# Optimization experiments

Hardware: AMD Instinct MI355X
Metric: run time of the kernel (lower is better)

The kernel has to match this reference:

```python
import jax, jax.numpy as jnp
import numpy as np
import math

D = 256; H = 8; DH = 32; FF = 2048; L = 6; B = 4; S = 1022


def _pe(n, d):
    pos = np.arange(n)[:, None]
    div = np.exp(np.arange(0, d, 2) * (-math.log(10000.0) / d))
    pe = np.zeros((n, d), np.float32)
    pe[:, 0::2] = np.sin(pos * div)
    pe[:, 1::2] = np.cos(pos * div)
    return jnp.asarray(pe)


def _ln(x, g, b):
    mu = x.mean(-1, keepdims=True)
    v = ((x - mu) ** 2).mean(-1, keepdims=True)
    return (x - mu) / jnp.sqrt(v + 1e-5) * g + b


def _forward(x, cls1, cls2, Wqkv, bqkv, Wo, bo, ln1_g, ln1_b, W1, b1, W2, b2, ln2_g, ln2_b, idx, pad):
    n = x.shape[1] + 2  # insert cls1 and cls2 tokens
    h = jnp.stack([jnp.concatenate([cls1, x[i, :idx[i]], cls2, x[i, idx[i]:]], axis=0) for i in range(B)])
    h = h + _pe(n, D)[None]  # [B,N,D]
    # block-diagonal two-segment mask per sample (additive bias form)
    pos = np.arange(n)
    bias = []
    for i in range(B):
        v1 = pos <= idx[i]
        v2 = (pos > idx[i]) & (pos < n - pad[i])
        allowed = np.outer(v1, v1) | np.outer(v2, v2)
        bias.append(np.where(allowed, 0.0, -1e9).astype(np.float32))
    bias = jnp.asarray(np.stack(bias))[:, None]  # [B,1,N,N]
    scale = 1.0 / math.sqrt(DH)
    for l in range(L):
        qkv = h @ Wqkv[l].T + bqkv[l]  # [B,N,3D]
        q, k, v = jnp.split(qkv, 3, axis=-1)
        q = q.reshape(B, n, H, DH).transpose(0, 2, 1, 3)
        k = k.reshape(B, n, H, DH).transpose(0, 2, 1, 3)
        v = v.reshape(B, n, H, DH).transpose(0, 2, 1, 3)
        scores = jnp.einsum('bhqd,bhkd->bhqk', q, k) * scale + bias
        p = jax.nn.softmax(scores, axis=-1)
        a = jnp.einsum('bhqk,bhkd->bhqd', p, v).transpose(0, 2, 1, 3).reshape(B, n, D)
        h = _ln(h + a @ Wo[l].T + bo[l], ln1_g[l], ln1_b[l])
        ff = jax.nn.relu(h @ W1[l].T + b1[l]) @ W2[l].T + b2[l]
        h = _ln(h + ff, ln2_g[l], ln2_b[l])
    # cls token outputs: position 0 (cls1) and position idx+1 (cls2)
    return jnp.stack([jnp.stack([h[i, 0], h[i, idx[i] + 1]]) for i in range(B)])  # [4,2,256]


def setup_inputs():
    key = jax.random.key(0)
    ks = jax.random.split(key, 8)
    s = 0.02
    return {
        'x': jax.random.normal(ks[0], (B, S, D), jnp.float32),
        'mask': jnp.zeros((1,), jnp.bool_),  # unused by the original forward
        'indices': jnp.array([[500, 600, 400, 300], [0, 0, 0, 0]], jnp.int32),
        'cls1': jax.random.uniform(ks[1], (1, D), jnp.float32),
        'cls2': jax.random.uniform(ks[2], (1, D), jnp.float32),
        'Wqkv': jax.random.normal(ks[3], (L, 3 * D, D), jnp.float32) * s,
        'bqkv': jnp.zeros((L, 3 * D), jnp.float32),
        'Wo': jax.random.normal(ks[4], (L, D, D), jnp.float32) * s,
        'bo': jnp.zeros((L, D), jnp.float32),
        'ln1_g': jnp.ones((L, D), jnp.float32),
        'ln1_b': jnp.zeros((L, D), jnp.float32),
        'W1': jax.random.normal(ks[5], (L, FF, D), jnp.float32) * s,
        'b1': jnp.zeros((L, FF), jnp.float32),
        'W2': jax.random.normal(ks[6], (L, D, FF), jnp.float32) * s,
        'b2': jnp.zeros((L, D), jnp.float32),
        'ln2_g': jnp.ones((L, D), jnp.float32),
        'ln2_b': jnp.zeros((L, D), jnp.float32),
    }


def reference(x, mask, indices, cls1, cls2, Wqkv, bqkv, Wo, bo, ln1_g, ln1_b, W1, b1, W2, b2, ln2_g, ln2_b):
    ind = np.asarray(indices)
    idx = [int(t) for t in ind[0]]
    pad = [int(t) for t in ind[1]]
    return _forward(x, cls1, cls2, Wqkv, bqkv, Wo, bo, ln1_g, ln1_b, W1, b1, W2, b2, ln2_g, ln2_b, idx, pad)
```

## Files before the change

kernel.cpp:

```cpp
#include <hip/hip_runtime.h>
#include <hip/hip_bf16.h>
#include <math.h>

typedef __hip_bfloat16 bf16;
typedef short bf16x8 __attribute__((ext_vector_type(8)));
typedef short short4v __attribute__((ext_vector_type(4)));
typedef float f32x4 __attribute__((ext_vector_type(4)));

#define D_MODEL 256
#define NTOK 1024
#define SEQ 1022
#define BATCH 4
#define NLAYER 6

__device__ inline void gload_lds16(const void* g, void* l) {
    __builtin_amdgcn_global_load_lds(
        (const __attribute__((address_space(1))) void*)g,
        (__attribute__((address_space(3))) void*)l, 16, 0, 0);
}

__global__ __launch_bounds__(256) void cast4_kernel(
    const float* __restrict__ s0, bf16* __restrict__ d0,
    const float* __restrict__ s1, bf16* __restrict__ d1,
    const float* __restrict__ s2, bf16* __restrict__ d2,
    const float* __restrict__ s3, bf16* __restrict__ d3)
{
    const int bid = blockIdx.x;
    const float* s; bf16* d; int base;
    if (bid < 1152)      { s = s0; d = d0; base = bid; }
    else if (bid < 1536) { s = s1; d = d1; base = bid - 1152; }
    else if (bid < 4608) { s = s2; d = d2; base = bid - 1536; }
    else                 { s = s3; d = d3; base = bid - 4608; }
    const int i = (base * 256 + threadIdx.x) * 4;
    f32x4 v = *(const f32x4*)(s + i);
    d[i + 0] = __float2bfloat16(v[0]);
    d[i + 1] = __float2bfloat16(v[1]);
    d[i + 2] = __float2bfloat16(v[2]);
    d[i + 3] = __float2bfloat16(v[3]);
}

__global__ __launch_bounds__(256) void embed_kernel(
    const float* __restrict__ x, const float* __restrict__ cls1,
    const float* __restrict__ cls2, const int* __restrict__ ind,
    float* __restrict__ h, bf16* __restrict__ hb)
{
    int i = blockIdx.x * 256 + threadIdx.x;
    int d = i & 255;
    int pos = (i >> 8) & 1023;
    int b = i >> 18;
    int idx = ind[b];
    float v;
    if (pos == 0) v = cls1[d];
    else if (pos == idx + 1) v = cls2[d];
    else if (pos <= idx) v = x[(b * SEQ + pos - 1) * D_MODEL + d];
    else v = x[(b * SEQ + pos - 2) * D_MODEL + d];
    int p = d >> 1;
    float freq = expf(-(float)p * (logf(10000.0f) / 128.0f));
    float ang = (float)pos * freq;
    v += (d & 1) ? cosf(ang) : sinf(ang);
    h[i] = v;
    hb[i] = __float2bfloat16(v);
}

template<int MR, int NR, int RELU, int HAS_RES, int WF32, int WBF16, int WVT, int SPLITK>
__global__ __launch_bounds__(256) void mfma_gemm(
    const bf16* __restrict__ A, const bf16* __restrict__ W,
    const float* __restrict__ bias, const float* __restrict__ R,
    float* __restrict__ Cf, bf16* __restrict__ Cb, bf16* __restrict__ vTb,
    int M, int N, int K)
{
    constexpr int BM = MR * 32, BN = NR * 32;
    constexpr int ACH = BM * 4;
    constexpr int BCH = BN * 4;
    __shared__ bf16 As[2][BM * 32];
    __shared__ bf16 Bs[2][BN * 32];
    const int ntile = N / BN;
    const int tiles = (M / BM) * ntile;
    const int ks = (SPLITK > 1) ? (blockIdx.x / tiles) : 0;
    const int bidt = (SPLITK > 1) ? (blockIdx.x % tiles) : blockIdx.x;
    const int bx = bidt % ntile, by = bidt / ntile;
    const int row0 = by * BM, col0 = bx * BN;
    const int KS = K / SPLITK;
    const int kbase = ks * KS;
    const int tid = threadIdx.x, lane = tid & 63, wave = tid >> 6;
    const int wr = wave >> 1, wc = wave & 1;
    const int l15 = lane & 15, l4 = lane >> 4;

    f32x4 acc[MR][NR];
    #pragma unroll
    for (int m = 0; m < MR; ++m)
        #pragma unroll
        for (int n = 0; n < NR; ++n) acc[m][n] = (f32x4)0.0f;

    const int nk = KS / 32;

    auto stage = [&](int buf, int t) {
        const int k0 = kbase + t * 32;
        #pragma unroll
        for (int p = 0; p < ACH / 256; ++p) {
            const int cbase = p * 256 + wave * 64;
            const int chunk = cbase + lane;
            const int r = chunk >> 2, c = chunk & 3;
            gload_lds16(A + (size_t)(row0 + r) * K + k0 + c * 8, &As[buf][cbase * 8]);
        }
        #pragma unroll
        for (int p = 0; p < BCH / 256; ++p) {
            const int cbase = p * 256 + wave * 64;
            const int chunk = cbase + lane;
            const int r = chunk >> 2, c = chunk & 3;
            gload_lds16(W + (size_t)(col0 + r) * K + k0 + c * 8, &Bs[buf][cbase * 8]);
        }
    };

    stage(0, 0);
    __syncthreads();
    int cur = 0;
    for (int t = 0; t < nk; ++t) {
        if (t + 1 < nk) stage(cur ^ 1, t + 1);
        bf16x8 af[MR], bfr[NR];
        #pragma unroll
        for (int m = 0; m < MR; ++m)
            af[m] = *(const bf16x8*)&As[cur][(wr * MR * 16 + m * 16 + l15) * 32 + l4 * 8];
        #pragma unroll
        for (int n = 0; n < NR; ++n)
            bfr[n] = *(const bf16x8*)&Bs[cur][(wc * NR * 16 + n * 16 + l15) * 32 + l4 * 8];
        #pragma unroll
        for (int m = 0; m < MR; ++m)
            #pragma unroll
            for (int n = 0; n < NR; ++n)
                acc[m][n] = __builtin_amdgcn_mfma_f32_16x16x32_bf16(af[m], bfr[n], acc[m][n], 0, 0, 0);
        __syncthreads();
        cur ^= 1;
    }

    #pragma unroll
    for (int m = 0; m < MR; ++m) {
        #pragma unroll
        for (int n = 0; n < NR; ++n) {
            const int col = col0 + wc * NR * 16 + n * 16 + l15;
            const float bv = (SPLITK > 1) ? 0.0f : bias[col];
            #pragma unroll
            for (int r = 0; r < 4; ++r) {
                const int row = row0 + wr * MR * 16 + m * 16 + l4 * 4 + r;
                float v = acc[m][n][r] + bv;
                if (HAS_RES) v += R[(size_t)row * N + col];
                if (RELU) v = fmaxf(v, 0.0f);
                if (WF32) Cf[(size_t)ks * M * N + (size_t)row * N + col] = v;
                if (WBF16) {
                    if (WVT && col >= 512) {
                        const int hh = (col >> 5) - 16, d = col & 31;
                        const int bb = row >> 10, tt = row & 1023;
                        vTb[(((size_t)bb * 8 + hh) * 32 + d) * 1024 + tt] = __float2bfloat16(v);
                    } else {
                        Cb[(size_t)row * N + col] = __float2bfloat16(v);
                    }
                }
            }
        }
    }
}

template<int K>
__global__ __launch_bounds__(512) void gemm256_ln8_kernel(
    const bf16* __restrict__ A, const bf16* __restrict__ W,
    const float* __restrict__ bias, const float* __restrict__ g,
    const float* __restrict__ be, float* __restrict__ h, bf16* __restrict__ hb)
{
    constexpr int KW = K / 8;
    constexpr int NSTEP = KW / 32;
    __shared__ float part[4][16][260];
    const int tid = threadIdx.x, lane = tid & 63, wave = tid >> 6;
    const int l15 = lane & 15, l4 = lane >> 4;
    const int row0 = blockIdx.x * 16;

    f32x4 acc[16];
    #pragma unroll
    for (int n = 0; n < 16; ++n) acc[n] = (f32x4)0.0f;
    #pragma unroll
    for (int s = 0; s < NSTEP; ++s) {
        const int kk = wave * KW + s * 32;
        const bf16x8 af = *(const bf16x8*)(A + (size_t)(row0 + l15) * K + kk + l4 * 8);
        #pragma unroll
        for (int n = 0; n < 16; ++n) {
            const bf16x8 bfr = *(const bf16x8*)(W + (size_t)(n * 16 + l15) * K + kk + l4 * 8);
            acc[n] = __builtin_amdgcn_mfma_f32_16x16x32_bf16(af, bfr, acc[n], 0, 0, 0);
        }
    }
    if (wave < 4) {
        #pragma unroll
        for (int n = 0; n < 16; ++n)
            #pragma unroll
            for (int r = 0; r < 4; ++r)
                part[wave][l4 * 4 + r][n * 16 + l15] = acc[n][r];
    }
    __syncthreads();
    if (wave >= 4) {
        #pragma unroll
        for (int n = 0; n < 16; ++n)
            #pragma unroll
            for (int r = 0; r < 4; ++r)
                part[wave - 4][l4 * 4 + r][n * 16 + l15] += acc[n][r];
    }
    __syncthreads();

    const int row = tid >> 5, c8 = (tid & 31) * 8;
    f32x4 v0 = *(const f32x4*)&part[0][row][c8];
    f32x4 v1 = *(const f32x4*)&part[0][row][c8 + 4];
    #pragma unroll
    for (int w = 1; w < 4; ++w) {
        v0 += *(const f32x4*)&part[w][row][c8];
        v1 += *(const f32x4*)&part[w][row][c8 + 4];
    }
    float* hrow = h + (size_t)(row0 + row) * 256 + c8;
    v0 += *(const f32x4*)(bias + c8)     + *(const f32x4*)(hrow);
    v1 += *(const f32x4*)(bias + c8 + 4) + *(const f32x4*)(hrow + 4);
    float s1 = (v0[0] + v0[1]) + (v0[2] + v0[3]) + (v1[0] + v1[1]) + (v1[2] + v1[3]);
    #pragma unroll
    for (int off = 16; off >= 1; off >>= 1) s1 += __shfl_xor(s1, off);
    const float mu = s1 * (1.0f / 256.0f);
    float s2 = 0.0f;
    #pragma unroll
    for (int q = 0; q < 4; ++q) { float d0 = v0[q] - mu, d1 = v1[q] - mu; s2 += d0 * d0 + d1 * d1; }
    #pragma unroll
    for (int off = 16; off >= 1; off >>= 1) s2 += __shfl_xor(s2, off);
    const float inv = 1.0f / sqrtf(s2 * (1.0f / 256.0f) + 1e-5f);
    short* hbrow = (short*)hb + (size_t)(row0 + row) * 256 + c8;
    const f32x4 gv0 = *(const f32x4*)(g + c8),  gv1 = *(const f32x4*)(g + c8 + 4);
    const f32x4 ev0 = *(const f32x4*)(be + c8), ev1 = *(const f32x4*)(be + c8 + 4);
    f32x4 y0, y1; short4v p0, p1;
    #pragma unroll
    for (int q = 0; q < 4; ++q) {
        y0[q] = (v0[q] - mu) * inv * gv0[q] + ev0[q];
        y1[q] = (v1[q] - mu) * inv * gv1[q] + ev1[q];
        p0[q] = __builtin_bit_cast(short, __float2bfloat16(y0[q]));
        p1[q] = __builtin_bit_cast(short, __float2bfloat16(y1[q]));
    }
    *(f32x4*)(hrow) = y0;  *(f32x4*)(hrow + 4) = y1;
    *(short4v*)(hbrow) = p0;  *(short4v*)(hbrow + 4) = p1;
}

__global__ __launch_bounds__(256) void ln_merge_kernel(
    const float* __restrict__ P0, const float* __restrict__ P1,
    const float* __restrict__ bias, const float* __restrict__ g,
    const float* __restrict__ bb, float* __restrict__ h, bf16* __restrict__ hb)
{
    const int row = blockIdx.x * 4 + (threadIdx.x >> 6);
    const int lane = threadIdx.x & 63;
    const size_t off = (size_t)row * 256 + lane * 4;
    f32x4 xv = *(const f32x4*)(P0 + off);
    xv += *(const f32x4*)(P1 + off);
    xv += *(const f32x4*)(bias + lane * 4);
    xv += *(const f32x4*)(h + off);
    float s = (xv[0] + xv[1]) + (xv[2] + xv[3]);
    #pragma unroll
    for (int o = 32; o >= 1; o >>= 1) s += __shfl_xor(s, o);
    const float mu = s * (1.0f / 256.0f);
    f32x4 dv;
    float s2 = 0.0f;
    #pragma unroll
    for (int e = 0; e < 4; ++e) { dv[e] = xv[e] - mu; s2 += dv[e] * dv[e]; }
    #pragma unroll
    for (int o = 32; o >= 1; o >>= 1) s2 += __shfl_xor(s2, o);
    const float inv = 1.0f / sqrtf(s2 * (1.0f / 256.0f) + 1e-5f);
    const f32x4 gv = *(const f32x4*)(g + lane * 4);
    const f32x4 bv = *(const f32x4*)(bb + lane * 4);
    f32x4 y;
    short4v pk;
    #pragma unroll
    for (int e = 0; e < 4; ++e) {
        y[e] = dv[e] * inv * gv[e] + bv[e];
        pk[e] = __builtin_bit_cast(short, __float2bfloat16(y[e]));
    }
    *(f32x4*)(h + off) = y;
    *(short4v*)((short*)hb + off) = pk;
}

__global__ __launch_bounds__(256) void attn_mfma_kernel(
    const bf16* __restrict__ qkvb, const bf16* __restrict__ vT,
    bf16* __restrict__ att, const int* __restrict__ ind)
{
    __shared__ bf16 Ps[4][16][72];
    __shared__ float Opart[4][64][8];
    __shared__ float MLpart[4][64][8];
    const int qt = blockIdx.x & 31;
    const int hh = (blockIdx.x >> 5) & 7;
    const int b  = blockIdx.x >> 8;
    const int idx = ind[b];
    const int segEnd = NTOK - ind[4 + b];
    const int tid = threadIdx.x, lane = tid & 63, wave = tid >> 6;
    const int strip = wave >> 1, kh = wave & 1;
    const int l15 = lane & 15, l4 = lane >> 4;
    const int q0 = qt * 32 + strip * 16;
    const size_t tokbase = (size_t)b * NTOK;
    const bf16* vTh = vT + (((size_t)b * 8 + hh) * 32) * 1024;
    const float scale = 0.17677669529663687f;

    const bf16x8 qfrag = *(const bf16x8*)(qkvb + (tokbase + q0 + l15) * 768 + hh * 32 + l4 * 8);

    f32x4 acc_o[2];
    acc_o[0] = (f32x4)0.0f; acc_o[1] = (f32x4)0.0f;
    float mrun[4], lrun[4];
    bool v1q[4], v2q[4];
    #pragma unroll
    for (int r = 0; r < 4; ++r) {
        mrun[r] = -1e30f; lrun[r] = 0.0f;
        const int qg = q0 + l4 * 4 + r;
        v1q[r] = (qg <= idx);
        v2q[r] = (qg > idx) && (qg < segEnd);
    }

    const int kbeg = (q0 <= idx) ? 0 : (idx + 1);
    const int kend = (q0 + 15 > idx) ? segEnd : (idx + 1);
    const int t0 = kbeg & ~63;
    const int T = (kend - t0 + 63) >> 6;
    const int i0 = kh ? (T >> 1) : 0;
    const int i1 = kh ? T : (T >> 1);

    for (int i = i0; i < i1; ++i) {
        const int k0 = t0 + (i << 6);
        f32x4 sc[4];
        #pragma unroll
        for (int kt = 0; kt < 4; ++kt) {
            const bf16x8 kf = *(const bf16x8*)
                (qkvb + (tokbase + k0 + kt * 16 + l15) * 768 + 256 + hh * 32 + l4 * 8);
            sc[kt] = __builtin_amdgcn_mfma_f32_16x16x32_bf16(qfrag, kf, (f32x4)0.0f, 0, 0, 0);
        }
        float mloc[4] = {-1e30f, -1e30f, -1e30f, -1e30f};
        #pragma unroll
        for (int kt = 0; kt < 4; ++kt) {
            const int k = k0 + kt * 16 + l15;
            const bool v1k = (k <= idx);
            const bool v2k = (k > idx) && (k < segEnd);
            #pragma unroll
            for (int r = 0; r < 4; ++r) {
                const bool ok = (v1q[r] && v1k) || (v2q[r] && v2k);
                const float s = ok ? sc[kt][r] * scale : -1e30f;
                sc[kt][r] = s;
                mloc[r] = fmaxf(mloc[r], s);
            }
        }
        #pragma unroll
        for (int r = 0; r < 4; ++r) {
            mloc[r] = fmaxf(mloc[r], __shfl_xor(mloc[r], 1));
            mloc[r] = fmaxf(mloc[r], __shfl_xor(mloc[r], 2));
            mloc[r] = fmaxf(mloc[r], __shfl_xor(mloc[r], 4));
            mloc[r] = fmaxf(mloc[r], __shfl_xor(mloc[r], 8));
            const float mnew = fmaxf(mrun[r], mloc[r]);
            const float c = __expf(mrun[r] - mnew);
            mrun[r] = mnew;
            mloc[r] = c;
        }
        float psum[4] = {0.0f, 0.0f, 0.0f, 0.0f};
        #pragma unroll
        for (int kt = 0; kt < 4; ++kt) {
            #pragma unroll
            for (int r = 0; r < 4; ++r) {
                const float s = sc[kt][r];
                const float p = (s > -5e29f) ? __expf(s - mrun[r]) : 0.0f;
                psum[r] += p;
                Ps[wave][l4 * 4 + r][kt * 16 + l15] = __float2bfloat16(p);
            }
        }
        #pragma unroll
        for (int r = 0; r < 4; ++r) {
            float ps = psum[r];
            ps += __shfl_xor(ps, 1); ps += __shfl_xor(ps, 2);
            ps += __shfl_xor(ps, 4); ps += __shfl_xor(ps, 8);
            lrun[r] = lrun[r] * mloc[r] + ps;
            acc_o[0][r] *= mloc[r];
            acc_o[1][r] *= mloc[r];
        }
        #pragma unroll
        for (int ks = 0; ks < 2; ++ks) {
            const bf16x8 pa = *(const bf16x8*)&Ps[wave][l15][ks * 32 + l4 * 8];
            #pragma unroll
            for (int dt = 0; dt < 2; ++dt) {
                const bf16x8 vb = *(const bf16x8*)
                    (vTh + (size_t)(dt * 16 + l15) * 1024 + k0 + ks * 32 + l4 * 8);
                acc_o[dt] = __builtin_amdgcn_mfma_f32_16x16x32_bf16(pa, vb, acc_o[dt], 0, 0, 0);
            }
        }
    }

    #pragma unroll
    for (int r = 0; r < 4; ++r) {
        Opart[wave][lane][r]     = acc_o[0][r];
        Opart[wave][lane][4 + r] = acc_o[1][r];
        MLpart[wave][lane][r]     = mrun[r];
        MLpart[wave][lane][4 + r] = lrun[r];
    }
    __syncthreads();
    if (kh == 0) {
        #pragma unroll
        for (int r = 0; r < 4; ++r) {
            const float m1 = MLpart[wave + 1][lane][r];
            const float l1 = MLpart[wave + 1][lane][4 + r];
            const float ms = fmaxf(mrun[r], m1);
            const float c0 = __expf(mrun[r] - ms);
            const float c1 = __expf(m1 - ms);
            const float lt = lrun[r] * c0 + l1 * c1;
            const float invl = (lt > 0.0f) ? (1.0f / lt) : 0.0f;
            const float o0 = (acc_o[0][r] * c0 + Opart[wave + 1][lane][r] * c1) * invl;
            const float o1 = (acc_o[1][r] * c0 + Opart[wave + 1][lane][4 + r] * c1) * invl;
            const int qg = q0 + l4 * 4 + r;
            bf16* op = att + (tokbase + qg) * 256 + hh * 32 + l15;
            op[0]  = __float2bfloat16(o0);
            op[16] = __float2bfloat16(o1);
        }
    }
}

__global__ __launch_bounds__(256) void gather_kernel(
    const float* __restrict__ h, const int* __restrict__ ind, float* __restrict__ out)
{
    int b = blockIdx.x;
    int tid = threadIdx.x;
    out[(b * 2 + 0) * 256 + tid] = h[(b * NTOK + 0) * 256 + tid];
    out[(b * 2 + 1) * 256 + tid] = h[(b * NTOK + ind[b] + 1) * 256 + tid];
}

extern "C" void kernel_launch(void* const* d_in, const int* in_sizes, int n_in,
                              void* d_out, int out_size, void* d_ws, size_t ws_size,
                              hipStream_t stream)
{
    const float* x    = (const float*)d_in[0];
    const int*   ind  = (const int*)d_in[2];
    const float* cls1 = (const float*)d_in[3];
    const float* cls2 = (const float*)d_in[4];
    const float* Wqkv = (const float*)d_in[5];
    const float* bqkv = (const float*)d_in[6];
    const float* Wo   = (const float*)d_in[7];
    const float* bo   = (const float*)d_in[8];
    const float* g1   = (const float*)d_in[9];
    const float* be1  = (const float*)d_in[10];
    const float* W1   = (const float*)d_in[11];
    const float* bf1  = (const float*)d_in[12];
    const float* W2   = (const float*)d_in[13];
    const float* bf2  = (const float*)d_in[14];
    const float* g2   = (const float*)d_in[15];
    const float* be2  = (const float*)d_in[16];
    float* out = (float*)d_out;

    float* ws   = (float*)d_ws;
    float* h    = ws;
    float* tmp2 = h + 1048576;
    bf16* hb    = (bf16*)(tmp2 + 2097152);
    bf16* qkvb  = hb + 1048576;
    bf16* vTb   = qkvb + 3145728;
    bf16* attb  = vTb + 1048576;
    bf16* ffb   = attb + 1048576;
    bf16* wqkvb = ffb + 8388608;
    bf16* wob   = wqkvb + 1179648;
    bf16* w1b   = wob + 393216;
    bf16* w2b   = w1b + 3145728;

    const int M = BATCH * NTOK;

    cast4_kernel<<<7680, 256, 0, stream>>>(Wqkv, wqkvb, Wo, wob, W1, w1b, W2, w2b);
    embed_kernel<<<M, 256, 0, stream>>>(x, cls1, cls2, ind, h, hb);

    for (int l = 0; l < NLAYER; ++l) {
        const bf16*  Wqkv_l = wqkvb + (size_t)l * 196608;
        const float* bqkv_l = bqkv + (size_t)l * 768;
        const bf16*  Wo_l   = wob + (size_t)l * 65536;
        const float* bo_l   = bo + (size_t)l * 256;
        const float* g1_l   = g1 + (size_t)l * 256;
        const float* be1_l  = be1 + (size_t)l * 256;
        const bf16*  W1_l   = w1b + (size_t)l * 524288;
        const float* b1_l   = bf1 + (size_t)l * 2048;
        const bf16*  W2_l   = w2b + (size_t)l * 524288;
        const float* b2_l   = bf2 + (size_t)l * 256;
        const float* g2_l   = g2 + (size_t)l * 256;
        const float* be2_l  = be2 + (size_t)l * 256;

        mfma_gemm<2, 4, 0, 0, 0, 1, 1, 1><<<(M / 64) * (768 / 128), 256, 0, stream>>>(
            hb, Wqkv_l, bqkv_l, nullptr, nullptr, qkvb, vTb, M, 768, 256);
        attn_mfma_kernel<<<BATCH * 8 * 32, 256, 0, stream>>>(qkvb, vTb, attb, ind);
        gemm256_ln8_kernel<256><<<M / 16, 512, 0, stream>>>(
            attb, Wo_l, bo_l, g1_l, be1_l, h, hb);
        mfma_gemm<4, 4, 1, 0, 0, 1, 0, 1><<<(M / 128) * (2048 / 128), 256, 0, stream>>>(
            hb, W1_l, b1_l, nullptr, nullptr, ffb, nullptr, M, 2048, 256);
        mfma_gemm<2, 2, 0, 0, 1, 0, 0, 2><<<2 * (M / 64) * (256 / 64), 256, 0, stream>>>(
            ffb, W2_l, nullptr, nullptr, tmp2, nullptr, nullptr, M, 256, 2048);
        ln_merge_kernel<<<M / 4, 256, 0, stream>>>(
            tmp2, tmp2 + (size_t)M * 256, b2_l, g2_l, be2_l, h, hb);
    }

    gather_kernel<<<BATCH, 256, 0, stream>>>(h, ind, out);
}
```

Before: 485.9 us.

## Fuse attention with Wo projection and LayerNorm into one kernel

```diff
diff --git a/kernel.cpp b/kernel.cpp
--- a/kernel.cpp
+++ b/kernel.cpp
@@ -160,137 +160,22 @@
     }
 }
 
-template<int K>
-__global__ __launch_bounds__(512) void gemm256_ln8_kernel(
-    const bf16* __restrict__ A, const bf16* __restrict__ W,
-    const float* __restrict__ bias, const float* __restrict__ g,
-    const float* __restrict__ be, float* __restrict__ h, bf16* __restrict__ hb)
-{
-    constexpr int KW = K / 8;
-    constexpr int NSTEP = KW / 32;
+__global__ __launch_bounds__(512) void attn_wo_ln_kernel(
+    const bf16* __restrict__ qkvb, const bf16* __restrict__ vT,
+    const bf16* __restrict__ Wo, const float* __restrict__ bo,
+    const float* __restrict__ g, const float* __restrict__ be,
+    float* __restrict__ h, bf16* __restrict__ hb, const int* __restrict__ ind)
+{
+    __shared__ bf16 Ps[8][16][72];
+    __shared__ bf16 att_s[16][264];
     __shared__ float part[4][16][260];
-    const int tid = threadIdx.x, lane = tid & 63, wave = tid >> 6;
-    const int l15 = lane & 15, l4 = lane >> 4;
-    const int row0 = blockIdx.x * 16;
-
-    f32x4 acc[16];
-    #pragma unroll
-    for (int n = 0; n < 16; ++n) acc[n] = (f32x4)0.0f;
-    #pragma unroll
-    for (int s = 0; s < NSTEP; ++s) {
-        const int kk = wave * KW + s * 32;
-        const bf16x8 af = *(const bf16x8*)(A + (size_t)(row0 + l15) * K + kk + l4 * 8);
-        #pragma unroll
-        for (int n = 0; n < 16; ++n) {
-            const bf16x8 bfr = *(const bf16x8*)(W + (size_t)(n * 16 + l15) * K + kk + l4 * 8);
-            acc[n] = __builtin_amdgcn_mfma_f32_16x16x32_bf16(af, bfr, acc[n], 0, 0, 0);
-        }
-    }
-    if (wave < 4) {
-        #pragma unroll
-        for (int n = 0; n < 16; ++n)
-            #pragma unroll
-            for (int r = 0; r < 4; ++r)
-                part[wave][l4 * 4 + r][n * 16 + l15] = acc[n][r];
-    }
-    __syncthreads();
-    if (wave >= 4) {
-        #pragma unroll
-        for (int n = 0; n < 16; ++n)
-            #pragma unroll
-            for (int r = 0; r < 4; ++r)
-                part[wave - 4][l4 * 4 + r][n * 16 + l15] += acc[n][r];
-    }
-    __syncthreads();
-
-    const int row = tid >> 5, c8 = (tid & 31) * 8;
-    f32x4 v0 = *(const f32x4*)&part[0][row][c8];
-    f32x4 v1 = *(const f32x4*)&part[0][row][c8 + 4];
-    #pragma unroll
-    for (int w = 1; w < 4; ++w) {
-        v0 += *(const f32x4*)&part[w][row][c8];
-        v1 += *(const f32x4*)&part[w][row][c8 + 4];
-    }
-    float* hrow = h + (size_t)(row0 + row) * 256 + c8;
-    v0 += *(const f32x4*)(bias + c8)     + *(const f32x4*)(hrow);
-    v1 += *(const f32x4*)(bias + c8 + 4) + *(const f32x4*)(hrow + 4);
-    float s1 = (v0[0] + v0[1]) + (v0[2] + v0[3]) + (v1[0] + v1[1]) + (v1[2] + v1[3]);
-    #pragma unroll
-    for (int off = 16; off >= 1; off >>= 1) s1 += __shfl_xor(s1, off);
-    const float mu = s1 * (1.0f / 256.0f);
-    float s2 = 0.0f;
-    #pragma unroll
-    for (int q = 0; q < 4; ++q) { float d0 = v0[q] - mu, d1 = v1[q] - mu; s2 += d0 * d0 + d1 * d1; }
-    #pragma unroll
-    for (int off = 16; off >= 1; off >>= 1) s2 += __shfl_xor(s2, off);
-    const float inv = 1.0f / sqrtf(s2 * (1.0f / 256.0f) + 1e-5f);
-    short* hbrow = (short*)hb + (size_t)(row0 + row) * 256 + c8;
-    const f32x4 gv0 = *(const f32x4*)(g + c8),  gv1 = *(const f32x4*)(g + c8 + 4);
-    const f32x4 ev0 = *(const f32x4*)(be + c8), ev1 = *(const f32x4*)(be + c8 + 4);
-    f32x4 y0, y1; short4v p0, p1;
-    #pragma unroll
-    for (int q = 0; q < 4; ++q) {
-        y0[q] = (v0[q] - mu) * inv * gv0[q] + ev0[q];
-        y1[q] = (v1[q] - mu) * inv * gv1[q] + ev1[q];
-        p0[q] = __builtin_bit_cast(short, __float2bfloat16(y0[q]));
-        p1[q] = __builtin_bit_cast(short, __float2bfloat16(y1[q]));
-    }
-    *(f32x4*)(hrow) = y0;  *(f32x4*)(hrow + 4) = y1;
-    *(short4v*)(hbrow) = p0;  *(short4v*)(hbrow + 4) = p1;
-}
-
-__global__ __launch_bounds__(256) void ln_merge_kernel(
-    const float* __restrict__ P0, const float* __restrict__ P1,
-    const float* __restrict__ bias, const float* __restrict__ g,
-    const float* __restrict__ bb, float* __restrict__ h, bf16* __restrict__ hb)
-{
-    const int row = blockIdx.x * 4 + (threadIdx.x >> 6);
-    const int lane = threadIdx.x & 63;
-    const size_t off = (size_t)row * 256 + lane * 4;
-    f32x4 xv = *(const f32x4*)(P0 + off);
-    xv += *(const f32x4*)(P1 + off);
-    xv += *(const f32x4*)(bias + lane * 4);
-    xv += *(const f32x4*)(h + off);
-    float s = (xv[0] + xv[1]) + (xv[2] + xv[3]);
-    #pragma unroll
-    for (int o = 32; o >= 1; o >>= 1) s += __shfl_xor(s, o);
-    const float mu = s * (1.0f / 256.0f);
-    f32x4 dv;
-    float s2 = 0.0f;
-    #pragma unroll
-    for (int e = 0; e < 4; ++e) { dv[e] = xv[e] - mu; s2 += dv[e] * dv[e]; }
-    #pragma unroll
-    for (int o = 32; o >= 1; o >>= 1) s2 += __shfl_xor(s2, o);
-    const float inv = 1.0f / sqrtf(s2 * (1.0f / 256.0f) + 1e-5f);
-    const f32x4 gv = *(const f32x4*)(g + lane * 4);
-    const f32x4 bv = *(const f32x4*)(bb + lane * 4);
-    f32x4 y;
-    short4v pk;
-    #pragma unroll
-    for (int e = 0; e < 4; ++e) {
-        y[e] = dv[e] * inv * gv[e] + bv[e];
-        pk[e] = __builtin_bit_cast(short, __float2bfloat16(y[e]));
-    }
-    *(f32x4*)(h + off) = y;
-    *(short4v*)((short*)hb + off) = pk;
-}
-
-__global__ __launch_bounds__(256) void attn_mfma_kernel(
-    const bf16* __restrict__ qkvb, const bf16* __restrict__ vT,
-    bf16* __restrict__ att, const int* __restrict__ ind)
-{
-    __shared__ bf16 Ps[4][16][72];
-    __shared__ float Opart[4][64][8];
-    __shared__ float MLpart[4][64][8];
-    const int qt = blockIdx.x & 31;
-    const int hh = (blockIdx.x >> 5) & 7;
-    const int b  = blockIdx.x >> 8;
+    const int qt = blockIdx.x & 63;
+    const int b  = blockIdx.x >> 6;
     const int idx = ind[b];
     const int segEnd = NTOK - ind[4 + b];
-    const int tid = threadIdx.x, lane = tid & 63, wave = tid >> 6;
-    const int strip = wave >> 1, kh = wave & 1;
+    const int tid = threadIdx.x, lane = tid & 63, hh = tid >> 6;
     const int l15 = lane & 15, l4 = lane >> 4;
-    const int q0 = qt * 32 + strip * 16;
+    const int q0 = qt * 16;
     const size_t tokbase = (size_t)b * NTOK;
     const bf16* vTh = vT + (((size_t)b * 8 + hh) * 32) * 1024;
     const float scale = 0.17677669529663687f;
@@ -311,13 +196,8 @@
 
     const int kbeg = (q0 <= idx) ? 0 : (idx + 1);
     const int kend = (q0 + 15 > idx) ? segEnd : (idx + 1);
-    const int t0 = kbeg & ~63;
-    const int T = (kend - t0 + 63) >> 6;
-    const int i0 = kh ? (T >> 1) : 0;
-    const int i1 = kh ? T : (T >> 1);
-
-    for (int i = i0; i < i1; ++i) {
-        const int k0 = t0 + (i << 6);
+
+    for (int k0 = (kbeg & ~63); k0 < kend; k0 += 64) {
         f32x4 sc[4];
         #pragma unroll
         for (int kt = 0; kt < 4; ++kt) {
@@ -358,7 +238,7 @@
                 const float s = sc[kt][r];
                 const float p = (s > -5e29f) ? __expf(s - mrun[r]) : 0.0f;
                 psum[r] += p;
-                Ps[wave][l4 * 4 + r][kt * 16 + l15] = __float2bfloat16(p);
+                Ps[hh][l4 * 4 + r][kt * 16 + l15] = __float2bfloat16(p);
             }
         }
         #pragma unroll
@@ -372,7 +252,7 @@
         }
         #pragma unroll
         for (int ks = 0; ks < 2; ++ks) {
-            const bf16x8 pa = *(const bf16x8*)&Ps[wave][l15][ks * 32 + l4 * 8];
+            const bf16x8 pa = *(const bf16x8*)&Ps[hh][l15][ks * 32 + l4 * 8];
             #pragma unroll
             for (int dt = 0; dt < 2; ++dt) {
                 const bf16x8 vb = *(const bf16x8*)
@@ -384,30 +264,111 @@
 
     #pragma unroll
     for (int r = 0; r < 4; ++r) {
-        Opart[wave][lane][r]     = acc_o[0][r];
-        Opart[wave][lane][4 + r] = acc_o[1][r];
-        MLpart[wave][lane][r]     = mrun[r];
-        MLpart[wave][lane][4 + r] = lrun[r];
+        const float invl = (lrun[r] > 0.0f) ? (1.0f / lrun[r]) : 0.0f;
+        att_s[l4 * 4 + r][hh * 32 + l15]      = __float2bfloat16(acc_o[0][r] * invl);
+        att_s[l4 * 4 + r][hh * 32 + 16 + l15] = __float2bfloat16(acc_o[1][r] * invl);
     }
     __syncthreads();
-    if (kh == 0) {
-        #pragma unroll
-        for (int r = 0; r < 4; ++r) {
-            const float m1 = MLpart[wave + 1][lane][r];
-            const float l1 = MLpart[wave + 1][lane][4 + r];
-            const float ms = fmaxf(mrun[r], m1);
-            const float c0 = __expf(mrun[r] - ms);
-            const float c1 = __expf(m1 - ms);
-            const float lt = lrun[r] * c0 + l1 * c1;
-            const float invl = (lt > 0.0f) ? (1.0f / lt) : 0.0f;
-            const float o0 = (acc_o[0][r] * c0 + Opart[wave + 1][lane][r] * c1) * invl;
-            const float o1 = (acc_o[1][r] * c0 + Opart[wave + 1][lane][4 + r] * c1) * invl;
-            const int qg = q0 + l4 * 4 + r;
-            bf16* op = att + (tokbase + qg) * 256 + hh * 32 + l15;
-            op[0]  = __float2bfloat16(o0);
-            op[16] = __float2bfloat16(o1);
-        }
-    }
+
+    f32x4 wacc[16];
+    #pragma unroll
+    for (int n = 0; n < 16; ++n) wacc[n] = (f32x4)0.0f;
+    {
+        const bf16x8 af = *(const bf16x8*)&att_s[l15][hh * 32 + l4 * 8];
+        #pragma unroll
+        for (int n = 0; n < 16; ++n) {
+            const bf16x8 bfr = *(const bf16x8*)(Wo + (size_t)(n * 16 + l15) * 256 + hh * 32 + l4 * 8);
+            wacc[n] = __builtin_amdgcn_mfma_f32_16x16x32_bf16(af, bfr, wacc[n], 0, 0, 0);
+        }
+    }
+    if (hh < 4) {
+        #pragma unroll
+        for (int n = 0; n < 16; ++n)
+            #pragma unroll
+            for (int r = 0; r < 4; ++r)
+                part[hh][l4 * 4 + r][n * 16 + l15] = wacc[n][r];
+    }
+    __syncthreads();
+    if (hh >= 4) {
+        #pragma unroll
+        for (int n = 0; n < 16; ++n)
+            #pragma unroll
+            for (int r = 0; r < 4; ++r)
+                part[hh - 4][l4 * 4 + r][n * 16 + l15] += wacc[n][r];
+    }
+    __syncthreads();
+
+    const int row = tid >> 5, c8 = (tid & 31) * 8;
+    f32x4 v0, v1;
+    v0 = *(const f32x4*)&part[0][row][c8];
+    v1 = *(const f32x4*)&part[0][row][c8 + 4];
+    #pragma unroll
+    for (int w = 1; w < 4; ++w) {
+        v0 += *(const f32x4*)&part[w][row][c8];
+        v1 += *(const f32x4*)&part[w][row][c8 + 4];
+    }
+    float* hrow = h + (tokbase + q0 + row) * 256 + c8;
+    v0 += *(const f32x4*)(bo + c8)     + *(const f32x4*)(hrow);
+    v1 += *(const f32x4*)(bo + c8 + 4) + *(const f32x4*)(hrow + 4);
+    float s1 = (v0[0] + v0[1]) + (v0[2] + v0[3]) + (v1[0] + v1[1]) + (v1[2] + v1[3]);
+    #pragma unroll
+    for (int off = 16; off >= 1; off >>= 1) s1 += __shfl_xor(s1, off);
+    const float mu = s1 * (1.0f / 256.0f);
+    float s2 = 0.0f;
+    #pragma unroll
+    for (int q = 0; q < 4; ++q) { float d0 = v0[q] - mu, d1 = v1[q] - mu; s2 += d0 * d0 + d1 * d1; }
+    #pragma unroll
+    for (int off = 16; off >= 1; off >>= 1) s2 += __shfl_xor(s2, off);
+    const float inv = 1.0f / sqrtf(s2 * (1.0f / 256.0f) + 1e-5f);
+    short* hbrow = (short*)hb + (tokbase + q0 + row) * 256 + c8;
+    const f32x4 gv0 = *(const f32x4*)(g + c8),  gv1 = *(const f32x4*)(g + c8 + 4);
+    const f32x4 ev0 = *(const f32x4*)(be + c8), ev1 = *(const f32x4*)(be + c8 + 4);
+    f32x4 y0, y1; short4v p0, p1;
+    #pragma unroll
+    for (int q = 0; q < 4; ++q) {
+        y0[q] = (v0[q] - mu) * inv * gv0[q] + ev0[q];
+        y1[q] = (v1[q] - mu) * inv * gv1[q] + ev1[q];
+        p0[q] = __builtin_bit_cast(short, __float2bfloat16(y0[q]));
+        p1[q] = __builtin_bit_cast(short, __float2bfloat16(y1[q]));
+    }
+    *(f32x4*)(hrow) = y0;  *(f32x4*)(hrow + 4) = y1;
+    *(short4v*)(hbrow) = p0;  *(short4v*)(hbrow + 4) = p1;
+}
+
+__global__ __launch_bounds__(256) void ln_merge_kernel(
+    const float* __restrict__ P0, const float* __restrict__ P1,
+    const float* __restrict__ bias, const float* __restrict__ g,
+    const float* __restrict__ bb, float* __restrict__ h, bf16* __restrict__ hb)
+{
+    const int row = blockIdx.x * 4 + (threadIdx.x >> 6);
+    const int lane = threadIdx.x & 63;
+    const size_t off = (size_t)row * 256 + lane * 4;
+    f32x4 xv = *(const f32x4*)(P0 + off);
+    xv += *(const f32x4*)(P1 + off);
+    xv += *(const f32x4*)(bias + lane * 4);
+    xv += *(const f32x4*)(h + off);
+    float s = (xv[0] + xv[1]) + (xv[2] + xv[3]);
+    #pragma unroll
+    for (int o = 32; o >= 1; o >>= 1) s += __shfl_xor(s, o);
+    const float mu = s * (1.0f / 256.0f);
+    f32x4 dv;
+    float s2 = 0.0f;
+    #pragma unroll
+    for (int e = 0; e < 4; ++e) { dv[e] = xv[e] - mu; s2 += dv[e] * dv[e]; }
+    #pragma unroll
+    for (int o = 32; o >= 1; o >>= 1) s2 += __shfl_xor(s2, o);
+    const float inv = 1.0f / sqrtf(s2 * (1.0f / 256.0f) + 1e-5f);
+    const f32x4 gv = *(const f32x4*)(g + lane * 4);
+    const f32x4 bv = *(const f32x4*)(bb + lane * 4);
+    f32x4 y;
+    short4v pk;
+    #pragma unroll
+    for (int e = 0; e < 4; ++e) {
+        y[e] = dv[e] * inv * gv[e] + bv[e];
+        pk[e] = __builtin_bit_cast(short, __float2bfloat16(y[e]));
+    }
+    *(f32x4*)(h + off) = y;
+    *(short4v*)((short*)hb + off) = pk;
 }
 
 __global__ __launch_bounds__(256) void gather_kernel(
@@ -447,8 +408,7 @@
     bf16* hb    = (bf16*)(tmp2 + 2097152);
     bf16* qkvb  = hb + 1048576;
     bf16* vTb   = qkvb + 3145728;
-    bf16* attb  = vTb + 1048576;
-    bf16* ffb   = attb + 1048576;
+    bf16* ffb   = vTb + 1048576;
     bf16* wqkvb = ffb + 8388608;
     bf16* wob   = wqkvb + 1179648;
     bf16* w1b   = wob + 393216;
@@ -475,9 +435,8 @@
 
         mfma_gemm<2, 4, 0, 0, 0, 1, 1, 1><<<(M / 64) * (768 / 128), 256, 0, stream>>>(
             hb, Wqkv_l, bqkv_l, nullptr, nullptr, qkvb, vTb, M, 768, 256);
-        attn_mfma_kernel<<<BATCH * 8 * 32, 256, 0, stream>>>(qkvb, vTb, attb, ind);
-        gemm256_ln8_kernel<256><<<M / 16, 512, 0, stream>>>(
-            attb, Wo_l, bo_l, g1_l, be1_l, h, hb);
+        attn_wo_ln_kernel<<<BATCH * 64, 512, 0, stream>>>(
+            qkvb, vTb, Wo_l, bo_l, g1_l, be1_l, h, hb, ind);
         mfma_gemm<4, 4, 1, 0, 0, 1, 0, 1><<<(M / 128) * (2048 / 128), 256, 0, stream>>>(
             hb, W1_l, b1_l, nullptr, nullptr, ffb, nullptr, M, 2048, 256);
         mfma_gemm<2, 2, 0, 0, 1, 0, 0, 2><<<2 * (M / 64) * (256 / 64), 256, 0, stream>>>(
```

New measurement: 580.8 us. 1.2x slower.
